# Kernel optimization log

Measured on AMD Instinct MI355X. Metric: run time of the kernel, lower is better.

Reference implementation:

```python
import jax, jax.numpy as jnp
import numpy as np

NTYPE = 3
ALPHA = 0.2
E, N, H, D = 100000, 50000, 4, 128


def setup_inputs() -> dict:
    key = jax.random.key(0)
    k1, k2, k3 = jax.random.split(key, 3)
    batch = jax.random.randint(k1, (E, NTYPE), 0, N)
    # forward's broadcast (batch_features + aggregated) requires every node id
    # to appear at least once (torch.unique(batch) must have N entries)
    batch = batch.at[:N, 0].set(jnp.arange(N))
    batch_features = jax.random.normal(k2, (N, D), dtype=jnp.float32)
    att_weights = jax.random.normal(k3, (NTYPE * E, H, NTYPE - 1), dtype=jnp.float32)
    return {"batch": batch, "batch_features": batch_features, "att_weights": att_weights}


def reference(batch, batch_features, att_weights):
    n_nodes, d = batch_features.shape
    # feat block i: gather embeddings of all type-columns except i -> [NTYPE*E, NTYPE-1, D]
    feat = jnp.concatenate(
        [batch_features[batch[:, [j for j in range(NTYPE) if j != i]]] for i in range(NTYPE)],
        axis=0,
    )
    # batched attention matmul: [NTYPE*E, H, NTYPE-1] x [NTYPE*E, NTYPE-1, D] -> [NTYPE*E, H, D]
    att_feat = jnp.einsum('ehk,ekd->ehd', att_weights, feat)
    # block i of att_feat corresponds to node ids batch[:, i] (matches batch.T.flatten())
    batch_nodes = batch.T.reshape(-1)  # [NTYPE*E]
    # per-node scatter-max aggregation (torch.unique returns sorted ids 0..N-1)
    aggregated = jax.ops.segment_max(att_feat, batch_nodes, num_segments=n_nodes)  # [N, H, D]
    out = batch_features[:, None, :] + aggregated  # broadcast residual -> [N, H, D]
    out = jax.nn.leaky_relu(out, negative_slope=ALPHA)  # concat=True branch
    return out.reshape(n_nodes, -1)  # [N, H*D]
```

## Files before the change

kernel.cpp:

```cpp
#include <hip/hip_runtime.h>

#define NTYPE 3
#define H 4
#define D 128
#define ALPHA 0.2f
#define CAP 64
#define SCAN_TILE 1024

typedef float f2 __attribute__((ext_vector_type(2)));
typedef float f4 __attribute__((ext_vector_type(4)));
typedef int   i4 __attribute__((ext_vector_type(4)));

__global__ void scatter_direct_kernel(const int* __restrict__ batch,
                                      int* __restrict__ cnt,
                                      i4* __restrict__ recs, int E) {
    int r = blockIdx.x * blockDim.x + threadIdx.x;
    if (r >= E) return;
    const int* row = batch + 3 * r;
    int b0 = row[0], b1 = row[1], b2 = row[2];
    i4 v;
    int s0 = atomicAdd(&cnt[b0], 1);
    v.x = b1; v.y = b2; v.z = r; v.w = 0;
    __builtin_nontemporal_store(v, recs + (size_t)b0 * CAP + s0);
    int s1 = atomicAdd(&cnt[b1], 1);
    v.x = b0; v.y = b2; v.z = E + r;
    __builtin_nontemporal_store(v, recs + (size_t)b1 * CAP + s1);
    int s2 = atomicAdd(&cnt[b2], 1);
    v.x = b0; v.y = b1; v.z = 2 * E + r;
    __builtin_nontemporal_store(v, recs + (size_t)b2 * CAP + s2);
}

__global__ void __launch_bounds__(256)
aggregate_bucket_kernel(const float* __restrict__ bfeat,
                        const float* __restrict__ attw,
                        const i4* __restrict__ recs,
                        const int* __restrict__ cnt,
                        float* __restrict__ out, int N) {
    const int n = blockIdx.x * 4 + (threadIdx.x >> 6);
    if (n >= N) return;
    const int t = threadIdx.x & 63;
    const int d2 = 2 * t;
    const int e = cnt[n];
    const i4* bucket = recs + (size_t)n * CAP;

    const float NI = -__builtin_inff();
    f2 acc0 = {NI, NI}, acc1 = {NI, NI}, acc2 = {NI, NI}, acc3 = {NI, NI};

    int k = 0;
    for (; k + 2 <= e; k += 2) {
        const i4 ra = __builtin_nontemporal_load(bucket + k);
        const i4 rb = __builtin_nontemporal_load(bucket + k + 1);
        const f2 fa0 = *(const f2*)(bfeat + (size_t)ra.x * D + d2);
        const f2 fa1 = *(const f2*)(bfeat + (size_t)ra.y * D + d2);
        const f2 fb0 = *(const f2*)(bfeat + (size_t)rb.x * D + d2);
        const f2 fb1 = *(const f2*)(bfeat + (size_t)rb.y * D + d2);
        const f4 wa0 = __builtin_nontemporal_load((const f4*)(attw + (size_t)ra.z * 8));
        const f4 wa1 = __builtin_nontemporal_load((const f4*)(attw + (size_t)ra.z * 8 + 4));
        const f4 wb0 = __builtin_nontemporal_load((const f4*)(attw + (size_t)rb.z * 8));
        const f4 wb1 = __builtin_nontemporal_load((const f4*)(attw + (size_t)rb.z * 8 + 4));

        acc0.x = fmaxf(acc0.x, fmaf(wa0.x, fa0.x, wa0.y * fa1.x));
        acc0.y = fmaxf(acc0.y, fmaf(wa0.x, fa0.y, wa0.y * fa1.y));
        acc1.x = fmaxf(acc1.x, fmaf(wa0.z, fa0.x, wa0.w * fa1.x));
        acc1.y = fmaxf(acc1.y, fmaf(wa0.z, fa0.y, wa0.w * fa1.y));
        acc2.x = fmaxf(acc2.x, fmaf(wa1.x, fa0.x, wa1.y * fa1.x));
        acc2.y = fmaxf(acc2.y, fmaf(wa1.x, fa0.y, wa1.y * fa1.y));
        acc3.x = fmaxf(acc3.x, fmaf(wa1.z, fa0.x, wa1.w * fa1.x));
        acc3.y = fmaxf(acc3.y, fmaf(wa1.z, fa0.y, wa1.w * fa1.y));

        acc0.x = fmaxf(acc0.x, fmaf(wb0.x, fb0.x, wb0.y * fb1.x));
        acc0.y = fmaxf(acc0.y, fmaf(wb0.x, fb0.y, wb0.y * fb1.y));
        acc1.x = fmaxf(acc1.x, fmaf(wb0.z, fb0.x, wb0.w * fb1.x));
        acc1.y = fmaxf(acc1.y, fmaf(wb0.z, fb0.y, wb0.w * fb1.y));
        acc2.x = fmaxf(acc2.x, fmaf(wb1.x, fb0.x, wb1.y * fb1.x));
        acc2.y = fmaxf(acc2.y, fmaf(wb1.x, fb0.y, wb1.y * fb1.y));
        acc3.x = fmaxf(acc3.x, fmaf(wb1.z, fb0.x, wb1.w * fb1.x));
        acc3.y = fmaxf(acc3.y, fmaf(wb1.z, fb0.y, wb1.w * fb1.y));
    }
    if (k < e) {
        const i4 ra = __builtin_nontemporal_load(bucket + k);
        const f2 fa0 = *(const f2*)(bfeat + (size_t)ra.x * D + d2);
        const f2 fa1 = *(const f2*)(bfeat + (size_t)ra.y * D + d2);
        const f4 wa0 = __builtin_nontemporal_load((const f4*)(attw + (size_t)ra.z * 8));
        const f4 wa1 = __builtin_nontemporal_load((const f4*)(attw + (size_t)ra.z * 8 + 4));
        acc0.x = fmaxf(acc0.x, fmaf(wa0.x, fa0.x, wa0.y * fa1.x));
        acc0.y = fmaxf(acc0.y, fmaf(wa0.x, fa0.y, wa0.y * fa1.y));
        acc1.x = fmaxf(acc1.x, fmaf(wa0.z, fa0.x, wa0.w * fa1.x));
        acc1.y = fmaxf(acc1.y, fmaf(wa0.z, fa0.y, wa0.w * fa1.y));
        acc2.x = fmaxf(acc2.x, fmaf(wa1.x, fa0.x, wa1.y * fa1.x));
        acc2.y = fmaxf(acc2.y, fmaf(wa1.x, fa0.y, wa1.y * fa1.y));
        acc3.x = fmaxf(acc3.x, fmaf(wa1.z, fa0.x, wa1.w * fa1.x));
        acc3.y = fmaxf(acc3.y, fmaf(wa1.z, fa0.y, wa1.w * fa1.y));
    }

    const f2 br = *(const f2*)(bfeat + (size_t)n * D + d2);
    float* o = out + (size_t)n * (H * D) + d2;
    f2 v;
    v.x = br.x + acc0.x; v.y = br.y + acc0.y;
    v.x = v.x > 0.f ? v.x : ALPHA * v.x; v.y = v.y > 0.f ? v.y : ALPHA * v.y;
    __builtin_nontemporal_store(v, (f2*)(o + 0 * D));
    v.x = br.x + acc1.x; v.y = br.y + acc1.y;
    v.x = v.x > 0.f ? v.x : ALPHA * v.x; v.y = v.y > 0.f ? v.y : ALPHA * v.y;
    __builtin_nontemporal_store(v, (f2*)(o + 1 * D));
    v.x = br.x + acc2.x; v.y = br.y + acc2.y;
    v.x = v.x > 0.f ? v.x : ALPHA * v.x; v.y = v.y > 0.f ? v.y : ALPHA * v.y;
    __builtin_nontemporal_store(v, (f2*)(o + 2 * D));
    v.x = br.x + acc3.x; v.y = br.y + acc3.y;
    v.x = v.x > 0.f ? v.x : ALPHA * v.x; v.y = v.y > 0.f ? v.y : ALPHA * v.y;
    __builtin_nontemporal_store(v, (f2*)(o + 3 * D));
}

__global__ void count_kernel(const int* __restrict__ batch,
                             int* __restrict__ cnt,
                             int* __restrict__ rnk, int E) {
    int r = blockIdx.x * blockDim.x + threadIdx.x;
    if (r >= E) return;
    const int* row = batch + 3 * r;
    rnk[r]         = atomicAdd(&cnt[row[0]], 1);
    rnk[E + r]     = atomicAdd(&cnt[row[1]], 1);
    rnk[2 * E + r] = atomicAdd(&cnt[row[2]], 1);
}

__global__ void __launch_bounds__(256)
scan_kernel(int* __restrict__ cnt, unsigned long long* __restrict__ tstate, int N) {
    __shared__ int lds[256];
    __shared__ int excl_s;
    const int b = blockIdx.x;
    const int t = threadIdx.x;
    const int base = b * SCAN_TILE + t * 4;

    int4 v = make_int4(0, 0, 0, 0);
    if (base + 3 < N) v = *(const int4*)(cnt + base);
    else {
        if (base + 0 < N) v.x = cnt[base + 0];
        if (base + 1 < N) v.y = cnt[base + 1];
        if (base + 2 < N) v.z = cnt[base + 2];
    }
    const int s = v.x + v.y + v.z + v.w;

    lds[t] = s;
    __syncthreads();
    for (int off = 1; off < 256; off <<= 1) {
        int tv = (t >= off) ? lds[t - off] : 0;
        __syncthreads();
        lds[t] += tv;
        __syncthreads();
    }
    const int texcl = lds[t] - s;
    const int tsum  = lds[255];

    if (t == 0) {
        if (b == 0) {
            atomicExch(&tstate[0], (2ULL << 32) | (unsigned)tsum);
            excl_s = 0;
        } else {
            atomicExch(&tstate[b], (1ULL << 32) | (unsigned)tsum);
            int exclusive = 0;
            int p = b - 1;
            for (;;) {
                unsigned long long st;
                do { st = atomicAdd(&tstate[p], 0ULL); } while ((st >> 32) == 0);
                exclusive += (int)(unsigned)st;
                if ((st >> 32) == 2) break;
                --p;
            }
            atomicExch(&tstate[b], (2ULL << 32) | (unsigned)(exclusive + tsum));
            excl_s = exclusive;
        }
    }
    __syncthreads();
    const int excl = excl_s + texcl;

    int4 o;
    o.x = excl;
    o.y = excl + v.x;
    o.z = excl + v.x + v.y;
    o.w = excl + v.x + v.y + v.z;
    if (base + 3 < N) *(int4*)(cnt + base) = o;
    else {
        if (base + 0 < N) cnt[base + 0] = o.x;
        if (base + 1 < N) cnt[base + 1] = o.y;
        if (base + 2 < N) cnt[base + 2] = o.z;
    }
}

__global__ void scatter_idx_kernel(const int* __restrict__ batch,
                                   const int* __restrict__ start,
                                   const int* __restrict__ rnk,
                                   int4* __restrict__ recs, int E) {
    int r = blockIdx.x * blockDim.x + threadIdx.x;
    if (r >= E) return;
    const int* row = batch + 3 * r;
    int b0 = row[0], b1 = row[1], b2 = row[2];
    recs[start[b0] + rnk[r]]         = make_int4(b1, b2, r, 0);
    recs[start[b1] + rnk[E + r]]     = make_int4(b0, b2, E + r, 0);
    recs[start[b2] + rnk[2 * E + r]] = make_int4(b0, b1, 2 * E + r, 0);
}

__global__ void __launch_bounds__(64)
aggregate_idx_kernel(const float* __restrict__ bfeat,
                     const float* __restrict__ attw,
                     const int4* __restrict__ recs,
                     const int* __restrict__ cursor,
                     float* __restrict__ out, int M) {
    const int n = blockIdx.x;
    const int d2 = 2 * threadIdx.x;
    const int s = cursor[n];
    const int e = (n == (int)gridDim.x - 1) ? M : cursor[n + 1];

    const float NI = -__builtin_inff();
    f2 acc0 = {NI, NI}, acc1 = {NI, NI}, acc2 = {NI, NI}, acc3 = {NI, NI};

    for (int k = s; k < e; ++k) {
        const i4 ra = __builtin_nontemporal_load((const i4*)(recs + k));
        const f2 fa0 = *(const f2*)(bfeat + (size_t)ra.x * D + d2);
        const f2 fa1 = *(const f2*)(bfeat + (size_t)ra.y * D + d2);
        const f4 wa0 = __builtin_nontemporal_load((const f4*)(attw + (size_t)ra.z * 8));
        const f4 wa1 = __builtin_nontemporal_load((const f4*)(attw + (size_t)ra.z * 8 + 4));
        acc0.x = fmaxf(acc0.x, fmaf(wa0.x, fa0.x, wa0.y * fa1.x));
        acc0.y = fmaxf(acc0.y, fmaf(wa0.x, fa0.y, wa0.y * fa1.y));
        acc1.x = fmaxf(acc1.x, fmaf(wa0.z, fa0.x, wa0.w * fa1.x));
        acc1.y = fmaxf(acc1.y, fmaf(wa0.z, fa0.y, wa0.w * fa1.y));
        acc2.x = fmaxf(acc2.x, fmaf(wa1.x, fa0.x, wa1.y * fa1.x));
        acc2.y = fmaxf(acc2.y, fmaf(wa1.x, fa0.y, wa1.y * fa1.y));
        acc3.x = fmaxf(acc3.x, fmaf(wa1.z, fa0.x, wa1.w * fa1.x));
        acc3.y = fmaxf(acc3.y, fmaf(wa1.z, fa0.y, wa1.w * fa1.y));
    }

    const f2 br = *(const f2*)(bfeat + (size_t)n * D + d2);
    float* o = out + (size_t)n * (H * D) + d2;
    f2 v;
    v.x = br.x + acc0.x; v.y = br.y + acc0.y;
    v.x = v.x > 0.f ? v.x : ALPHA * v.x; v.y = v.y > 0.f ? v.y : ALPHA * v.y;
    __builtin_nontemporal_store(v, (f2*)(o + 0 * D));
    v.x = br.x + acc1.x; v.y = br.y + acc1.y;
    v.x = v.x > 0.f ? v.x : ALPHA * v.x; v.y = v.y > 0.f ? v.y : ALPHA * v.y;
    __builtin_nontemporal_store(v, (f2*)(o + 1 * D));
    v.x = br.x + acc2.x; v.y = br.y + acc2.y;
    v.x = v.x > 0.f ? v.x : ALPHA * v.x; v.y = v.y > 0.f ? v.y : ALPHA * v.y;
    __builtin_nontemporal_store(v, (f2*)(o + 2 * D));
    v.x = br.x + acc3.x; v.y = br.y + acc3.y;
    v.x = v.x > 0.f ? v.x : ALPHA * v.x; v.y = v.y > 0.f ? v.y : ALPHA * v.y;
    __builtin_nontemporal_store(v, (f2*)(o + 3 * D));
}

extern "C" void kernel_launch(void* const* d_in, const int* in_sizes, int n_in,
                              void* d_out, int out_size, void* d_ws, size_t ws_size,
                              hipStream_t stream) {
    const int* batch   = (const int*)d_in[0];
    const float* bfeat = (const float*)d_in[1];
    const float* attw  = (const float*)d_in[2];
    const int E = in_sizes[0] / NTYPE;
    const int N = in_sizes[1] / D;
    const int M = NTYPE * E;
    const int eb = (E + 255) / 256;

    int* cnt = (int*)d_ws;
    size_t boff = (((size_t)N * sizeof(int)) + 15) & ~(size_t)15;
    const size_t bucket_need = boff + (size_t)N * CAP * sizeof(int4);

    if (ws_size >= bucket_need) {
        i4* recs = (i4*)((char*)d_ws + boff);
        hipMemsetAsync(cnt, 0, sizeof(int) * (size_t)N, stream);
        scatter_direct_kernel<<<eb, 256, 0, stream>>>(batch, cnt, recs, E);
        aggregate_bucket_kernel<<<(N + 3) / 4, 256, 0, stream>>>(
            bfeat, attw, recs, cnt, (float*)d_out, N);
        return;
    }

    const int nb = (N + SCAN_TILE - 1) / SCAN_TILE;
    size_t off = (size_t)N * sizeof(int);
    off = (off + 7) & ~(size_t)7;
    unsigned long long* tstate = (unsigned long long*)((char*)d_ws + off);
    off += (size_t)nb * 8;
    off = (off + 15) & ~(size_t)15;
    const size_t zero_bytes = off;
    int4* recs = (int4*)((char*)d_ws + off);
    int* rnk = (int*)d_out;

    hipMemsetAsync(d_ws, 0, zero_bytes, stream);
    count_kernel<<<eb, 256, 0, stream>>>(batch, cnt, rnk, E);
    scan_kernel<<<nb, 256, 0, stream>>>(cnt, tstate, N);
    scatter_idx_kernel<<<eb, 256, 0, stream>>>(batch, cnt, rnk, recs, E);
    aggregate_idx_kernel<<<N, 64, 0, stream>>>(bfeat, attw, recs, cnt,
                                               (float*)d_out, M);
}
```

Measured before the change: 215.6 us.

## Replace fixed-capacity bucket path with CSR and grid-stride unrolled aggregation

Removes the fixed 64-slot per-node bucket scatter path and always builds compact CSR records via count, scan and scatter. The aggregation kernel becomes grid-stride over nodes with a capped grid and processes three records per iteration to expose more independent gathers. This avoids the padded bucket workspace and sparse record layout, but adds a scan kernel and an extra scatter pass in exchange.

```diff
diff --git a/kernel.cpp b/kernel.cpp
--- a/kernel.cpp
+++ b/kernel.cpp
@@ -4,111 +4,11 @@
 #define H 4
 #define D 128
 #define ALPHA 0.2f
-#define CAP 64
 #define SCAN_TILE 1024
 
 typedef float f2 __attribute__((ext_vector_type(2)));
 typedef float f4 __attribute__((ext_vector_type(4)));
 typedef int   i4 __attribute__((ext_vector_type(4)));
-
-__global__ void scatter_direct_kernel(const int* __restrict__ batch,
-                                      int* __restrict__ cnt,
-                                      i4* __restrict__ recs, int E) {
-    int r = blockIdx.x * blockDim.x + threadIdx.x;
-    if (r >= E) return;
-    const int* row = batch + 3 * r;
-    int b0 = row[0], b1 = row[1], b2 = row[2];
-    i4 v;
-    int s0 = atomicAdd(&cnt[b0], 1);
-    v.x = b1; v.y = b2; v.z = r; v.w = 0;
-    __builtin_nontemporal_store(v, recs + (size_t)b0 * CAP + s0);
-    int s1 = atomicAdd(&cnt[b1], 1);
-    v.x = b0; v.y = b2; v.z = E + r;
-    __builtin_nontemporal_store(v, recs + (size_t)b1 * CAP + s1);
-    int s2 = atomicAdd(&cnt[b2], 1);
-    v.x = b0; v.y = b1; v.z = 2 * E + r;
-    __builtin_nontemporal_store(v, recs + (size_t)b2 * CAP + s2);
-}
-
-__global__ void __launch_bounds__(256)
-aggregate_bucket_kernel(const float* __restrict__ bfeat,
-                        const float* __restrict__ attw,
-                        const i4* __restrict__ recs,
-                        const int* __restrict__ cnt,
-                        float* __restrict__ out, int N) {
-    const int n = blockIdx.x * 4 + (threadIdx.x >> 6);
-    if (n >= N) return;
-    const int t = threadIdx.x & 63;
-    const int d2 = 2 * t;
-    const int e = cnt[n];
-    const i4* bucket = recs + (size_t)n * CAP;
-
-    const float NI = -__builtin_inff();
-    f2 acc0 = {NI, NI}, acc1 = {NI, NI}, acc2 = {NI, NI}, acc3 = {NI, NI};
-
-    int k = 0;
-    for (; k + 2 <= e; k += 2) {
-        const i4 ra = __builtin_nontemporal_load(bucket + k);
-        const i4 rb = __builtin_nontemporal_load(bucket + k + 1);
-        const f2 fa0 = *(const f2*)(bfeat + (size_t)ra.x * D + d2);
-        const f2 fa1 = *(const f2*)(bfeat + (size_t)ra.y * D + d2);
-        const f2 fb0 = *(const f2*)(bfeat + (size_t)rb.x * D + d2);
-        const f2 fb1 = *(const f2*)(bfeat + (size_t)rb.y * D + d2);
-        const f4 wa0 = __builtin_nontemporal_load((const f4*)(attw + (size_t)ra.z * 8));
-        const f4 wa1 = __builtin_nontemporal_load((const f4*)(attw + (size_t)ra.z * 8 + 4));
-        const f4 wb0 = __builtin_nontemporal_load((const f4*)(attw + (size_t)rb.z * 8));
-        const f4 wb1 = __builtin_nontemporal_load((const f4*)(attw + (size_t)rb.z * 8 + 4));
-
-        acc0.x = fmaxf(acc0.x, fmaf(wa0.x, fa0.x, wa0.y * fa1.x));
-        acc0.y = fmaxf(acc0.y, fmaf(wa0.x, fa0.y, wa0.y * fa1.y));
-        acc1.x = fmaxf(acc1.x, fmaf(wa0.z, fa0.x, wa0.w * fa1.x));
-        acc1.y = fmaxf(acc1.y, fmaf(wa0.z, fa0.y, wa0.w * fa1.y));
-        acc2.x = fmaxf(acc2.x, fmaf(wa1.x, fa0.x, wa1.y * fa1.x));
-        acc2.y = fmaxf(acc2.y, fmaf(wa1.x, fa0.y, wa1.y * fa1.y));
-        acc3.x = fmaxf(acc3.x, fmaf(wa1.z, fa0.x, wa1.w * fa1.x));
-        acc3.y = fmaxf(acc3.y, fmaf(wa1.z, fa0.y, wa1.w * fa1.y));
-
-        acc0.x = fmaxf(acc0.x, fmaf(wb0.x, fb0.x, wb0.y * fb1.x));
-        acc0.y = fmaxf(acc0.y, fmaf(wb0.x, fb0.y, wb0.y * fb1.y));
-        acc1.x = fmaxf(acc1.x, fmaf(wb0.z, fb0.x, wb0.w * fb1.x));
-        acc1.y = fmaxf(acc1.y, fmaf(wb0.z, fb0.y, wb0.w * fb1.y));
-        acc2.x = fmaxf(acc2.x, fmaf(wb1.x, fb0.x, wb1.y * fb1.x));
-        acc2.y = fmaxf(acc2.y, fmaf(wb1.x, fb0.y, wb1.y * fb1.y));
-        acc3.x = fmaxf(acc3.x, fmaf(wb1.z, fb0.x, wb1.w * fb1.x));
-        acc3.y = fmaxf(acc3.y, fmaf(wb1.z, fb0.y, wb1.w * fb1.y));
-    }
-    if (k < e) {
-        const i4 ra = __builtin_nontemporal_load(bucket + k);
-        const f2 fa0 = *(const f2*)(bfeat + (size_t)ra.x * D + d2);
-        const f2 fa1 = *(const f2*)(bfeat + (size_t)ra.y * D + d2);
-        const f4 wa0 = __builtin_nontemporal_load((const f4*)(attw + (size_t)ra.z * 8));
-        const f4 wa1 = __builtin_nontemporal_load((const f4*)(attw + (size_t)ra.z * 8 + 4));
-        acc0.x = fmaxf(acc0.x, fmaf(wa0.x, fa0.x, wa0.y * fa1.x));
-        acc0.y = fmaxf(acc0.y, fmaf(wa0.x, fa0.y, wa0.y * fa1.y));
-        acc1.x = fmaxf(acc1.x, fmaf(wa0.z, fa0.x, wa0.w * fa1.x));
-        acc1.y = fmaxf(acc1.y, fmaf(wa0.z, fa0.y, wa0.w * fa1.y));
-        acc2.x = fmaxf(acc2.x, fmaf(wa1.x, fa0.x, wa1.y * fa1.x));
-        acc2.y = fmaxf(acc2.y, fmaf(wa1.x, fa0.y, wa1.y * fa1.y));
-        acc3.x = fmaxf(acc3.x, fmaf(wa1.z, fa0.x, wa1.w * fa1.x));
-        acc3.y = fmaxf(acc3.y, fmaf(wa1.z, fa0.y, wa1.w * fa1.y));
-    }
-
-    const f2 br = *(const f2*)(bfeat + (size_t)n * D + d2);
-    float* o = out + (size_t)n * (H * D) + d2;
-    f2 v;
-    v.x = br.x + acc0.x; v.y = br.y + acc0.y;
-    v.x = v.x > 0.f ? v.x : ALPHA * v.x; v.y = v.y > 0.f ? v.y : ALPHA * v.y;
-    __builtin_nontemporal_store(v, (f2*)(o + 0 * D));
-    v.x = br.x + acc1.x; v.y = br.y + acc1.y;
-    v.x = v.x > 0.f ? v.x : ALPHA * v.x; v.y = v.y > 0.f ? v.y : ALPHA * v.y;
-    __builtin_nontemporal_store(v, (f2*)(o + 1 * D));
-    v.x = br.x + acc2.x; v.y = br.y + acc2.y;
-    v.x = v.x > 0.f ? v.x : ALPHA * v.x; v.y = v.y > 0.f ? v.y : ALPHA * v.y;
-    __builtin_nontemporal_store(v, (f2*)(o + 2 * D));
-    v.x = br.x + acc3.x; v.y = br.y + acc3.y;
-    v.x = v.x > 0.f ? v.x : ALPHA * v.x; v.y = v.y > 0.f ? v.y : ALPHA * v.y;
-    __builtin_nontemporal_store(v, (f2*)(o + 3 * D));
-}
 
 __global__ void count_kernel(const int* __restrict__ batch,
                              int* __restrict__ cnt,
@@ -116,9 +16,10 @@
     int r = blockIdx.x * blockDim.x + threadIdx.x;
     if (r >= E) return;
     const int* row = batch + 3 * r;
-    rnk[r]         = atomicAdd(&cnt[row[0]], 1);
-    rnk[E + r]     = atomicAdd(&cnt[row[1]], 1);
-    rnk[2 * E + r] = atomicAdd(&cnt[row[2]], 1);
+    int b0 = row[0], b1 = row[1], b2 = row[2];
+    rnk[r]         = atomicAdd(&cnt[b0], 1);
+    rnk[E + r]     = atomicAdd(&cnt[b1], 1);
+    rnk[2 * E + r] = atomicAdd(&cnt[b2], 1);
 }
 
 __global__ void __launch_bounds__(256)
@@ -197,51 +98,92 @@
     recs[start[b2] + rnk[2 * E + r]] = make_int4(b0, b1, 2 * E + r, 0);
 }
 
+#define COMP(w0, w1, f0, f1)                                   \
+    acc0.x = fmaxf(acc0.x, fmaf(w0.x, f0.x, w0.y * f1.x));     \
+    acc0.y = fmaxf(acc0.y, fmaf(w0.x, f0.y, w0.y * f1.y));     \
+    acc1.x = fmaxf(acc1.x, fmaf(w0.z, f0.x, w0.w * f1.x));     \
+    acc1.y = fmaxf(acc1.y, fmaf(w0.z, f0.y, w0.w * f1.y));     \
+    acc2.x = fmaxf(acc2.x, fmaf(w1.x, f0.x, w1.y * f1.x));     \
+    acc2.y = fmaxf(acc2.y, fmaf(w1.x, f0.y, w1.y * f1.y));     \
+    acc3.x = fmaxf(acc3.x, fmaf(w1.z, f0.x, w1.w * f1.x));     \
+    acc3.y = fmaxf(acc3.y, fmaf(w1.z, f0.y, w1.w * f1.y));
+
 __global__ void __launch_bounds__(64)
-aggregate_idx_kernel(const float* __restrict__ bfeat,
-                     const float* __restrict__ attw,
-                     const int4* __restrict__ recs,
-                     const int* __restrict__ cursor,
-                     float* __restrict__ out, int M) {
-    const int n = blockIdx.x;
-    const int d2 = 2 * threadIdx.x;
-    const int s = cursor[n];
-    const int e = (n == (int)gridDim.x - 1) ? M : cursor[n + 1];
-
-    const float NI = -__builtin_inff();
-    f2 acc0 = {NI, NI}, acc1 = {NI, NI}, acc2 = {NI, NI}, acc3 = {NI, NI};
-
-    for (int k = s; k < e; ++k) {
-        const i4 ra = __builtin_nontemporal_load((const i4*)(recs + k));
-        const f2 fa0 = *(const f2*)(bfeat + (size_t)ra.x * D + d2);
-        const f2 fa1 = *(const f2*)(bfeat + (size_t)ra.y * D + d2);
-        const f4 wa0 = __builtin_nontemporal_load((const f4*)(attw + (size_t)ra.z * 8));
-        const f4 wa1 = __builtin_nontemporal_load((const f4*)(attw + (size_t)ra.z * 8 + 4));
-        acc0.x = fmaxf(acc0.x, fmaf(wa0.x, fa0.x, wa0.y * fa1.x));
-        acc0.y = fmaxf(acc0.y, fmaf(wa0.x, fa0.y, wa0.y * fa1.y));
-        acc1.x = fmaxf(acc1.x, fmaf(wa0.z, fa0.x, wa0.w * fa1.x));
-        acc1.y = fmaxf(acc1.y, fmaf(wa0.z, fa0.y, wa0.w * fa1.y));
-        acc2.x = fmaxf(acc2.x, fmaf(wa1.x, fa0.x, wa1.y * fa1.x));
-        acc2.y = fmaxf(acc2.y, fmaf(wa1.x, fa0.y, wa1.y * fa1.y));
-        acc3.x = fmaxf(acc3.x, fmaf(wa1.z, fa0.x, wa1.w * fa1.x));
-        acc3.y = fmaxf(acc3.y, fmaf(wa1.z, fa0.y, wa1.w * fa1.y));
-    }
-
-    const f2 br = *(const f2*)(bfeat + (size_t)n * D + d2);
-    float* o = out + (size_t)n * (H * D) + d2;
-    f2 v;
-    v.x = br.x + acc0.x; v.y = br.y + acc0.y;
-    v.x = v.x > 0.f ? v.x : ALPHA * v.x; v.y = v.y > 0.f ? v.y : ALPHA * v.y;
-    __builtin_nontemporal_store(v, (f2*)(o + 0 * D));
-    v.x = br.x + acc1.x; v.y = br.y + acc1.y;
-    v.x = v.x > 0.f ? v.x : ALPHA * v.x; v.y = v.y > 0.f ? v.y : ALPHA * v.y;
-    __builtin_nontemporal_store(v, (f2*)(o + 1 * D));
-    v.x = br.x + acc2.x; v.y = br.y + acc2.y;
-    v.x = v.x > 0.f ? v.x : ALPHA * v.x; v.y = v.y > 0.f ? v.y : ALPHA * v.y;
-    __builtin_nontemporal_store(v, (f2*)(o + 2 * D));
-    v.x = br.x + acc3.x; v.y = br.y + acc3.y;
-    v.x = v.x > 0.f ? v.x : ALPHA * v.x; v.y = v.y > 0.f ? v.y : ALPHA * v.y;
-    __builtin_nontemporal_store(v, (f2*)(o + 3 * D));
+aggregate_kernel(const float* __restrict__ bfeat,
+                 const float* __restrict__ attw,
+                 const i4* __restrict__ recs,
+                 const int* __restrict__ cursor,
+                 float* __restrict__ out, int N, int M) {
+    const int d2 = 2 * (int)threadIdx.x;
+
+    for (int n = blockIdx.x; n < N; n += gridDim.x) {
+        const int s = cursor[n];
+        const int e = (n == N - 1) ? M : cursor[n + 1];
+
+        const float NI = -__builtin_inff();
+        f2 acc0 = {NI, NI}, acc1 = {NI, NI}, acc2 = {NI, NI}, acc3 = {NI, NI};
+
+        int k = s;
+        for (; k + 3 <= e; k += 3) {
+            const i4 ra = __builtin_nontemporal_load(recs + k);
+            const i4 rb = __builtin_nontemporal_load(recs + k + 1);
+            const i4 rc = __builtin_nontemporal_load(recs + k + 2);
+            const f2 fa0 = *(const f2*)(bfeat + (size_t)ra.x * D + d2);
+            const f2 fa1 = *(const f2*)(bfeat + (size_t)ra.y * D + d2);
+            const f2 fb0 = *(const f2*)(bfeat + (size_t)rb.x * D + d2);
+            const f2 fb1 = *(const f2*)(bfeat + (size_t)rb.y * D + d2);
+            const f2 fc0 = *(const f2*)(bfeat + (size_t)rc.x * D + d2);
+            const f2 fc1 = *(const f2*)(bfeat + (size_t)rc.y * D + d2);
+            const f4 wa0 = __builtin_nontemporal_load((const f4*)(attw + (size_t)ra.z * 8));
+            const f4 wa1 = __builtin_nontemporal_load((const f4*)(attw + (size_t)ra.z * 8 + 4));
+            const f4 wb0 = __builtin_nontemporal_load((const f4*)(attw + (size_t)rb.z * 8));
+            const f4 wb1 = __builtin_nontemporal_load((const f4*)(attw + (size_t)rb.z * 8 + 4));
+            const f4 wc0 = __builtin_nontemporal_load((const f4*)(attw + (size_t)rc.z * 8));
+            const f4 wc1 = __builtin_nontemporal_load((const f4*)(attw + (size_t)rc.z * 8 + 4));
+            COMP(wa0, wa1, fa0, fa1)
+            COMP(wb0, wb1, fb0, fb1)
+            COMP(wc0, wc1, fc0, fc1)
+        }
+        if (k + 2 <= e) {
+            const i4 ra = __builtin_nontemporal_load(recs + k);
+            const i4 rb = __builtin_nontemporal_load(recs + k + 1);
+            const f2 fa0 = *(const f2*)(bfeat + (size_t)ra.x * D + d2);
+            const f2 fa1 = *(const f2*)(bfeat + (size_t)ra.y * D + d2);
+            const f2 fb0 = *(const f2*)(bfeat + (size_t)rb.x * D + d2);
+            const f2 fb1 = *(const f2*)(bfeat + (size_t)rb.y * D + d2);
+            const f4 wa0 = __builtin_nontemporal_load((const f4*)(attw + (size_t)ra.z * 8));
+            const f4 wa1 = __builtin_nontemporal_load((const f4*)(attw + (size_t)ra.z * 8 + 4));
+            const f4 wb0 = __builtin_nontemporal_load((const f4*)(attw + (size_t)rb.z * 8));
+            const f4 wb1 = __builtin_nontemporal_load((const f4*)(attw + (size_t)rb.z * 8 + 4));
+            COMP(wa0, wa1, fa0, fa1)
+            COMP(wb0, wb1, fb0, fb1)
+            k += 2;
+        }
+        if (k < e) {
+            const i4 ra = __builtin_nontemporal_load(recs + k);
+            const f2 fa0 = *(const f2*)(bfeat + (size_t)ra.x * D + d2);
+            const f2 fa1 = *(const f2*)(bfeat + (size_t)ra.y * D + d2);
+            const f4 wa0 = __builtin_nontemporal_load((const f4*)(attw + (size_t)ra.z * 8));
+            const f4 wa1 = __builtin_nontemporal_load((const f4*)(attw + (size_t)ra.z * 8 + 4));
+            COMP(wa0, wa1, fa0, fa1)
+        }
+
+        const f2 br = *(const f2*)(bfeat + (size_t)n * D + d2);
+        float* o = out + (size_t)n * (H * D) + d2;
+        f2 v;
+        v.x = br.x + acc0.x; v.y = br.y + acc0.y;
+        v.x = v.x > 0.f ? v.x : ALPHA * v.x; v.y = v.y > 0.f ? v.y : ALPHA * v.y;
+        __builtin_nontemporal_store(v, (f2*)(o + 0 * D));
+        v.x = br.x + acc1.x; v.y = br.y + acc1.y;
+        v.x = v.x > 0.f ? v.x : ALPHA * v.x; v.y = v.y > 0.f ? v.y : ALPHA * v.y;
+        __builtin_nontemporal_store(v, (f2*)(o + 1 * D));
+        v.x = br.x + acc2.x; v.y = br.y + acc2.y;
+        v.x = v.x > 0.f ? v.x : ALPHA * v.x; v.y = v.y > 0.f ? v.y : ALPHA * v.y;
+        __builtin_nontemporal_store(v, (f2*)(o + 2 * D));
+        v.x = br.x + acc3.x; v.y = br.y + acc3.y;
+        v.x = v.x > 0.f ? v.x : ALPHA * v.x; v.y = v.y > 0.f ? v.y : ALPHA * v.y;
+        __builtin_nontemporal_store(v, (f2*)(o + 3 * D));
+    }
 }
 
 extern "C" void kernel_launch(void* const* d_in, const int* in_sizes, int n_in,
@@ -253,35 +195,25 @@
     const int E = in_sizes[0] / NTYPE;
     const int N = in_sizes[1] / D;
     const int M = NTYPE * E;
+    const int nb = (N + SCAN_TILE - 1) / SCAN_TILE;
     const int eb = (E + 255) / 256;
 
-    int* cnt = (int*)d_ws;
-    size_t boff = (((size_t)N * sizeof(int)) + 15) & ~(size_t)15;
-    const size_t bucket_need = boff + (size_t)N * CAP * sizeof(int4);
-
-    if (ws_size >= bucket_need) {
-        i4* recs = (i4*)((char*)d_ws + boff);
-        hipMemsetAsync(cnt, 0, sizeof(int) * (size_t)N, stream);
-        scatter_direct_kernel<<<eb, 256, 0, stream>>>(batch, cnt, recs, E);
-        aggregate_bucket_kernel<<<(N + 3) / 4, 256, 0, stream>>>(
-            bfeat, attw, recs, cnt, (float*)d_out, N);
-        return;
-    }
-
-    const int nb = (N + SCAN_TILE - 1) / SCAN_TILE;
+    int* cursor = (int*)d_ws;
     size_t off = (size_t)N * sizeof(int);
     off = (off + 7) & ~(size_t)7;
     unsigned long long* tstate = (unsigned long long*)((char*)d_ws + off);
     off += (size_t)nb * 8;
     off = (off + 15) & ~(size_t)15;
     const size_t zero_bytes = off;
-    int4* recs = (int4*)((char*)d_ws + off);
+    i4* recs = (i4*)((char*)d_ws + off);
     int* rnk = (int*)d_out;
 
     hipMemsetAsync(d_ws, 0, zero_bytes, stream);
-    count_kernel<<<eb, 256, 0, stream>>>(batch, cnt, rnk, E);
-    scan_kernel<<<nb, 256, 0, stream>>>(cnt, tstate, N);
-    scatter_idx_kernel<<<eb, 256, 0, stream>>>(batch, cnt, rnk, recs, E);
-    aggregate_idx_kernel<<<N, 64, 0, stream>>>(bfeat, attw, recs, cnt,
-                                               (float*)d_out, M);
-}
+    count_kernel<<<eb, 256, 0, stream>>>(batch, cursor, rnk, E);
+    scan_kernel<<<nb, 256, 0, stream>>>(cursor, tstate, N);
+    scatter_idx_kernel<<<eb, 256, 0, stream>>>(batch, cursor, rnk, (int4*)recs, E);
+
+    int gb = N < 8192 ? N : 8192;
+    aggregate_kernel<<<gb, 64, 0, stream>>>(bfeat, attw, recs, cursor,
+                                            (float*)d_out, N, M);
+}
```

Result: faster. 201.7 us (-6.4%).
